# Performance work log

Hardware: AMD Instinct MI355X
Metric: run time of the kernel (lower is better)

The kernel has to match this reference:

```python
import jax, jax.numpy as jnp
import numpy as np

DILATIONS = [2 ** i for i in range(9)] * 3  # 27 layers
RD, SD, QD = 32, 512, 256


def conv1d(x, w, b, dilation=1, padding=0):
    # x: [B,C,T], w: [O,I,K], b: [O]
    out = jax.lax.conv_general_dilated(
        x, w, window_strides=(1,), padding=[(padding, padding)],
        rhs_dilation=(dilation,), dimension_numbers=('NCH', 'OIH', 'NCH'))
    return out + b[None, :, None]


def setup_inputs() -> dict:
    key = jax.random.key(0)
    ks = jax.random.split(key, 16)
    T = 131072
    L = len(DILATIONS)
    s = 0.05
    inp = {
        'x': jax.random.normal(ks[0], (1, 1, T), dtype=jnp.float32),
        'Wc': jax.random.normal(ks[1], (RD, 1, 3), dtype=jnp.float32) * s,
        'bc': jnp.zeros((RD,), dtype=jnp.float32),
        'Wt': jax.random.normal(ks[2], (L, RD, RD, 3), dtype=jnp.float32) * s,
        'bt': jnp.zeros((L, RD), dtype=jnp.float32),
        'Ws': jax.random.normal(ks[3], (L, RD, RD, 3), dtype=jnp.float32) * s,
        'bs': jnp.zeros((L, RD), dtype=jnp.float32),
        'Wskip': jax.random.normal(ks[4], (L, SD, RD, 1), dtype=jnp.float32) * s,
        'bskip': jnp.zeros((L, SD), dtype=jnp.float32),
        'Wdense': jax.random.normal(ks[5], (L, RD, RD, 1), dtype=jnp.float32) * s,
        'bdense': jnp.zeros((L, RD), dtype=jnp.float32),
        'Wp1': jax.random.normal(ks[6], (SD, SD, 1), dtype=jnp.float32) * s,
        'bp1': jnp.zeros((SD,), dtype=jnp.float32),
        'Wp2': jax.random.normal(ks[7], (QD, SD, 1), dtype=jnp.float32) * s,
        'bp2': jnp.zeros((QD,), dtype=jnp.float32),
    }
    return inp


def reference(x, Wc, bc, Wt, bt, Ws, bs, Wskip, bskip, Wdense, bdense, Wp1, bp1, Wp2, bp2):
    # causal conv: kernel 3, padding 1 (same length)
    x = conv1d(x, Wc, bc, dilation=1, padding=1)  # [1, RD, T]
    skip = jnp.zeros((1, SD, x.shape[2]), dtype=jnp.float32)
    for i, d in enumerate(DILATIONS):
        xin = x
        g = jnp.tanh(conv1d(x, Wt[i], bt[i], d, d)) * jax.nn.sigmoid(conv1d(x, Ws[i], bs[i], d, d))
        skip = skip + conv1d(g, Wskip[i], bskip[i])
        x = conv1d(g, Wdense[i], bdense[i]) + xin
    # NOTE: the original applies F.relu(x) on the residual path but then
    # overwrites x with the skip-path result, so that relu is dead code.
    out = conv1d(jax.nn.relu(conv1d(skip, Wp1, bp1)), Wp2, bp2)  # [1, QD, T]
    return jax.nn.log_softmax(out, axis=1)
```

## Files before the change

kernel.cpp:

```cpp
#include <hip/hip_runtime.h>

#define T_LEN 131072
#define RD 32
#define SD 512
#define QD 256
#define NL 27
#define KTOT (NL * RD)

typedef __attribute__((ext_vector_type(8))) short short8;
typedef __attribute__((ext_vector_type(4))) float floatx4;

__device__ __forceinline__ unsigned short f2bf(float f) {
    union { float f; unsigned int i; } v; v.f = f;
    unsigned int r = v.i + 0x7fffu + ((v.i >> 16) & 1u);
    return (unsigned short)(r >> 16);
}

__device__ __forceinline__ void gload_lds16(const void* g, void* l) {
    __builtin_amdgcn_global_load_lds(
        (const __attribute__((address_space(1))) unsigned int*)g,
        (__attribute__((address_space(3))) unsigned int*)l, 16, 0, 0);
}

__global__ __launch_bounds__(256)
void k_conv_init(const float* __restrict__ x, const float* __restrict__ Wc,
                 const float* __restrict__ bc, float* __restrict__ xout)
{
    const int t = blockIdx.x * 256 + threadIdx.x;
    const float xm = (t > 0) ? x[t - 1] : 0.f;
    const float x0 = x[t];
    const float xp = (t < T_LEN - 1) ? x[t + 1] : 0.f;
    float* row = xout + (size_t)t * RD;
#pragma unroll
    for (int o = 0; o < RD; ++o) {
        row[o] = bc[o] + Wc[o * 3 + 0] * xm + Wc[o * 3 + 1] * x0 + Wc[o * 3 + 2] * xp;
    }
}

__global__ __launch_bounds__(256)
void k_wprep(const float* __restrict__ Wt, const float* __restrict__ Ws,
             const float* __restrict__ Wd,
             unsigned short* __restrict__ Wg, unsigned short* __restrict__ Wdb)
{
    const int idx = blockIdx.x * 256 + threadIdx.x;
    const int n1 = NL * 64 * 96;
    const int n2 = NL * RD * RD;
    if (idx < n1) {
        const int l = idx / (64 * 96);
        const int rem = idx % (64 * 96);
        const int m = rem / 96;
        const int k = rem % 96;
        const int j = k / 32;
        const int c = k % 32;
        float v;
        if (m < 32) v = Wt[(((size_t)l * RD + m) * RD + c) * 3 + j];
        else        v = Ws[(((size_t)l * RD + (m - 32)) * RD + c) * 3 + j];
        Wg[idx] = f2bf(v);
    } else if (idx < n1 + n2) {
        const int i2 = idx - n1;
        Wdb[i2] = f2bf(Wd[i2]);
    }
}

__global__ __launch_bounds__(256)
void k_layer_mfma(const float* __restrict__ xin,
                  float* __restrict__ xout,
                  unsigned short* __restrict__ Gt,
                  const unsigned short* __restrict__ Wg,
                  const unsigned short* __restrict__ Wdb,
                  const float* __restrict__ bt, const float* __restrict__ bs,
                  const float* __restrict__ bd, int d, int layer)
{
    __shared__ unsigned short gtile[128 * 32];
    const int tid = threadIdx.x;
    const int lane = tid & 63;
    const int w = tid >> 6;
    const int quad = lane >> 4;
    const int l16 = lane & 15;
    const int tbase = blockIdx.x * 128 + w * 32;

    short8 afr[3][4];
#pragma unroll
    for (int j = 0; j < 3; ++j)
#pragma unroll
        for (int mt = 0; mt < 4; ++mt)
            afr[j][mt] = *reinterpret_cast<const short8*>(
                Wg + (size_t)(mt * 16 + l16) * 96 + j * 32 + quad * 8);

    floatx4 acc[4][2];
    const floatx4 vzero = {0.f, 0.f, 0.f, 0.f};
#pragma unroll
    for (int mt = 0; mt < 4; ++mt)
#pragma unroll
        for (int nt = 0; nt < 2; ++nt) acc[mt][nt] = vzero;

#pragma unroll
    for (int nt = 0; nt < 2; ++nt) {
        const int t = tbase + nt * 16 + l16;
#pragma unroll
        for (int j = 0; j < 3; ++j) {
            const int tt = t + (j - 1) * d;
            short8 b;
            if (tt >= 0 && tt < T_LEN) {
                const float* src = xin + (size_t)tt * RD + quad * 8;
                const floatx4 f0 = *reinterpret_cast<const floatx4*>(src);
                const floatx4 f1 = *reinterpret_cast<const floatx4*>(src + 4);
#pragma unroll
                for (int i = 0; i < 4; ++i) {
                    b[i] = (short)f2bf(f0[i]);
                    b[4 + i] = (short)f2bf(f1[i]);
                }
            } else {
#pragma unroll
                for (int i = 0; i < 8; ++i) b[i] = 0;
            }
#pragma unroll
            for (int mt = 0; mt < 4; ++mt)
                acc[mt][nt] = __builtin_amdgcn_mfma_f32_16x16x32_bf16(afr[j][mt], b, acc[mt][nt], 0, 0, 0);
        }
    }

#pragma unroll
    for (int nt = 0; nt < 2; ++nt) {
        const int t = tbase + nt * 16 + l16;
        const int tloc = w * 32 + nt * 16 + l16;
#pragma unroll
        for (int pair = 0; pair < 2; ++pair) {
            const floatx4 bt4 = *reinterpret_cast<const floatx4*>(bt + pair * 16 + quad * 4);
            const floatx4 bs4 = *reinterpret_cast<const floatx4*>(bs + pair * 16 + quad * 4);
            ushort4 u;
            unsigned short us[4];
#pragma unroll
            for (int r = 0; r < 4; ++r) {
                const float a1 = acc[pair][nt][r] + bt4[r];
                const float a2 = acc[2 + pair][nt][r] + bs4[r];
                const float th = 1.f - __fdividef(2.f, __expf(2.f * a1) + 1.f);
                const float sg = __fdividef(1.f, 1.f + __expf(-a2));
                us[r] = f2bf(th * sg);
            }
            u.x = us[0]; u.y = us[1]; u.z = us[2]; u.w = us[3];
            const int cbase = pair * 16 + quad * 4;
            *reinterpret_cast<ushort4*>(&gtile[tloc * 32 + cbase]) = u;
            *reinterpret_cast<ushort4*>(
                Gt + ((size_t)layer * T_LEN + t) * RD + cbase) = u;
        }
    }

    __syncthreads();

    short8 ad[2];
#pragma unroll
    for (int mt = 0; mt < 2; ++mt)
        ad[mt] = *reinterpret_cast<const short8*>(Wdb + (size_t)(mt * 16 + l16) * 32 + quad * 8);

#pragma unroll
    for (int nt = 0; nt < 2; ++nt) {
        const int t = tbase + nt * 16 + l16;
        const int tloc = w * 32 + nt * 16 + l16;
        const short8 bg = *reinterpret_cast<const short8*>(&gtile[tloc * 32 + quad * 8]);
#pragma unroll
        for (int mt = 0; mt < 2; ++mt) {
            const floatx4 a2 = __builtin_amdgcn_mfma_f32_16x16x32_bf16(ad[mt], bg, vzero, 0, 0, 0);
            const int m = mt * 16 + quad * 4;
            const floatx4 bd4 = *reinterpret_cast<const floatx4*>(bd + m);
            const floatx4 xi = *reinterpret_cast<const floatx4*>(xin + (size_t)t * RD + m);
            floatx4 o;
            o[0] = a2[0] + bd4[0] + xi[0];
            o[1] = a2[1] + bd4[1] + xi[1];
            o[2] = a2[2] + bd4[2] + xi[2];
            o[3] = a2[3] + bd4[3] + xi[3];
            *reinterpret_cast<floatx4*>(xout + (size_t)t * RD + m) = o;
        }
    }
}

__global__ __launch_bounds__(256)
void k_wcomb(const float* __restrict__ Wp1, const float* __restrict__ Wskip,
             unsigned short* __restrict__ Wcomb)
{
    const int idx = blockIdx.x * 256 + threadIdx.x;
    if (idx >= SD * KTOT) return;
    const int m = idx / KTOT;
    const int k = idx % KTOT;
    const int l = k / RD;
    const int c = k % RD;
    const float* wp1r = Wp1 + (size_t)m * SD;
    const float* wsk = Wskip + (size_t)l * SD * RD + c;
    float acc = 0.f;
    for (int j = 0; j < SD; ++j) acc += wp1r[j] * wsk[(size_t)j * RD];
    Wcomb[((size_t)l * SD + m) * RD + c] = f2bf(acc);
}

__global__ __launch_bounds__(512)
void k_hbias(const float* __restrict__ Wp1, const float* __restrict__ bp1,
             const float* __restrict__ bskip, float* __restrict__ hbias)
{
    __shared__ float sb[SD];
    const int tid = threadIdx.x;
    float s = 0.f;
    for (int l = 0; l < NL; ++l) s += bskip[l * SD + tid];
    sb[tid] = s;
    __syncthreads();
    float acc = bp1[tid];
    const float* r = Wp1 + (size_t)tid * SD;
    for (int j = 0; j < SD; ++j) acc += r[j] * sb[j];
    hbias[tid] = acc;
}

__global__ __launch_bounds__(256)
void k_cvt(const float* __restrict__ src, unsigned short* __restrict__ dst, int n)
{
    const int i = blockIdx.x * 256 + threadIdx.x;
    if (i < n) dst[i] = f2bf(src[i]);
}

__global__ __launch_bounds__(256)
void k_gemm1(const unsigned short* __restrict__ A,
             const unsigned short* __restrict__ B,
             const float* __restrict__ hbias,
             unsigned short* __restrict__ ht)
{
    __shared__ unsigned short ldsA[128 * 32];
    __shared__ unsigned short ldsB[128 * 32];
    const int tid = threadIdx.x;
    const int lane = tid & 63;
    const int w = tid >> 6;
    const int wm = w & 1;
    const int wn = w >> 1;
    const int quad = lane >> 4;
    const int l16 = lane & 15;

    const int g = blockIdx.x;
    const int m0 = ((g >> 3) & 3) * 128;
    const int n0 = ((g & 7) + 8 * (g >> 5)) * 128;

    const int r4 = lane >> 2;
    const int c4 = lane & 3;
    const int srcc = c4 ^ ((r4 >> 1) & 3);
    const int swz = (l16 >> 1) & 3;

    floatx4 acc[4][4];
    const floatx4 vzero = {0.f, 0.f, 0.f, 0.f};
#pragma unroll
    for (int mt = 0; mt < 4; ++mt)
#pragma unroll
        for (int nt = 0; nt < 4; ++nt) acc[mt][nt] = vzero;

    const unsigned short* pA = A + (size_t)(m0 + r4) * RD + srcc * 8;
    const unsigned short* pB = B + (size_t)(n0 + r4) * RD + srcc * 8;

    for (int kc = 0; kc < KTOT / 32; ++kc) {
#pragma unroll
        for (int c = 0; c < 2; ++c) {
            const int row = w * 32 + c * 16;
            gload_lds16(pA + ((size_t)kc * SD + row) * RD, &ldsA[(size_t)row * 32]);
            gload_lds16(pB + ((size_t)kc * T_LEN + row) * RD, &ldsB[(size_t)row * 32]);
        }
        __syncthreads();

        short8 afr[4], bfr[4];
#pragma unroll
        for (int mt = 0; mt < 4; ++mt)
            afr[mt] = *reinterpret_cast<const short8*>(
                &ldsA[(wm * 64 + mt * 16 + l16) * 32 + (quad ^ swz) * 8]);
#pragma unroll
        for (int nt = 0; nt < 4; ++nt)
            bfr[nt] = *reinterpret_cast<const short8*>(
                &ldsB[(wn * 64 + nt * 16 + l16) * 32 + (quad ^ swz) * 8]);
#pragma unroll
        for (int mt = 0; mt < 4; ++mt)
#pragma unroll
            for (int nt = 0; nt < 4; ++nt)
                acc[mt][nt] = __builtin_amdgcn_mfma_f32_16x16x32_bf16(afr[mt], bfr[nt], acc[mt][nt], 0, 0, 0);
        __syncthreads();
    }

#pragma unroll
    for (int mt = 0; mt < 4; ++mt) {
        const int m = m0 + wm * 64 + mt * 16 + quad * 4;
        const floatx4 hb = *reinterpret_cast<const floatx4*>(hbias + m);
        const size_t chunkbase = (size_t)(m >> 5) * T_LEN;
        const int mc = m & 31;
#pragma unroll
        for (int nt = 0; nt < 4; ++nt) {
            const int t = n0 + wn * 64 + nt * 16 + l16;
            ushort4 st;
            float v;
            v = acc[mt][nt][0] + hb[0]; st.x = f2bf(v > 0.f ? v : 0.f);
            v = acc[mt][nt][1] + hb[1]; st.y = f2bf(v > 0.f ? v : 0.f);
            v = acc[mt][nt][2] + hb[2]; st.z = f2bf(v > 0.f ? v : 0.f);
            v = acc[mt][nt][3] + hb[3]; st.w = f2bf(v > 0.f ? v : 0.f);
            *reinterpret_cast<ushort4*>(ht + (chunkbase + t) * RD + mc) = st;
        }
    }
}

__global__ __launch_bounds__(256)
void k_gemm2_lsm(const unsigned short* __restrict__ A,
                 const unsigned short* __restrict__ B,
                 const float* __restrict__ bp2,
                 float* __restrict__ out)
{
    __shared__ unsigned short ldsB[64 * 32];
    __shared__ float redmax[4 * 16 * 16];
    __shared__ float redsum[4 * 16 * 16];
    const int tid = threadIdx.x;
    const int lane = tid & 63;
    const int w = tid >> 6;
    const int quad = lane >> 4;
    const int l16 = lane & 15;
    const int m0 = w * 64;
    const int n0 = blockIdx.x * 64;

    const int r4 = lane >> 2;
    const int c4 = lane & 3;
    const int srcc = c4 ^ ((r4 >> 1) & 3);
    const int swz = (l16 >> 1) & 3;

    const unsigned short* ab[4];
#pragma unroll
    for (int mt = 0; mt < 4; ++mt)
        ab[mt] = A + (size_t)(m0 + mt * 16 + l16) * SD + quad * 8;

    const unsigned short* pB = B + (size_t)(n0 + w * 16 + r4) * RD + srcc * 8;

    floatx4 acc[4][4];
    const floatx4 vzero = {0.f, 0.f, 0.f, 0.f};
#pragma unroll
    for (int mt = 0; mt < 4; ++mt)
#pragma unroll
        for (int nt = 0; nt < 4; ++nt) acc[mt][nt] = vzero;

    for (int kc = 0; kc < SD / 32; ++kc) {
        const int k0 = kc * 32;
        gload_lds16(pB + (size_t)kc * T_LEN * RD, &ldsB[(size_t)(w * 16) * 32]);
        short8 afr[4];
#pragma unroll
        for (int mt = 0; mt < 4; ++mt)
            afr[mt] = *reinterpret_cast<const short8*>(ab[mt] + k0);
        __syncthreads();

        short8 bfr[4];
#pragma unroll
        for (int nt = 0; nt < 4; ++nt)
            bfr[nt] = *reinterpret_cast<const short8*>(
                &ldsB[(nt * 16 + l16) * 32 + (quad ^ swz) * 8]);
#pragma unroll
        for (int mt = 0; mt < 4; ++mt)
#pragma unroll
            for (int nt = 0; nt < 4; ++nt)
                acc[mt][nt] = __builtin_amdgcn_mfma_f32_16x16x32_bf16(
                    afr[mt], bfr[nt], acc[mt][nt], 0, 0, 0);
        __syncthreads();
    }

#pragma unroll
    for (int mt = 0; mt < 4; ++mt) {
        const int mb = m0 + mt * 16 + quad * 4;
        const floatx4 bz = *reinterpret_cast<const floatx4*>(bp2 + mb);
#pragma unroll
        for (int nt = 0; nt < 4; ++nt)
#pragma unroll
            for (int j = 0; j < 4; ++j) acc[mt][nt][j] += bz[j];
    }

#pragma unroll
    for (int nt = 0; nt < 4; ++nt) {
        float lm = -1e30f;
#pragma unroll
        for (int mt = 0; mt < 4; ++mt)
#pragma unroll
            for (int j = 0; j < 4; ++j) lm = fmaxf(lm, acc[mt][nt][j]);
        redmax[nt * 256 + l16 * 16 + w * 4 + quad] = lm;
    }
    __syncthreads();

    float lse[4];
#pragma unroll
    for (int nt = 0; nt < 4; ++nt) {
        float gm = -1e30f;
#pragma unroll
        for (int i = 0; i < 16; ++i) gm = fmaxf(gm, redmax[nt * 256 + l16 * 16 + i]);
        float ls = 0.f;
#pragma unroll
        for (int mt = 0; mt < 4; ++mt)
#pragma unroll
            for (int j = 0; j < 4; ++j) ls += __expf(acc[mt][nt][j] - gm);
        redsum[nt * 256 + l16 * 16 + w * 4 + quad] = ls;
        lse[nt] = gm;
    }
    __syncthreads();

#pragma unroll
    for (int nt = 0; nt < 4; ++nt) {
        float tot = 0.f;
#pragma unroll
        for (int i = 0; i < 16; ++i) tot += redsum[nt * 256 + l16 * 16 + i];
        lse[nt] = lse[nt] + __logf(tot);
    }

#pragma unroll
    for (int mt = 0; mt < 4; ++mt) {
        const int mb = m0 + mt * 16 + quad * 4;
#pragma unroll
        for (int nt = 0; nt < 4; ++nt) {
            const int t = n0 + nt * 16 + l16;
#pragma unroll
            for (int j = 0; j < 4; ++j)
                out[(size_t)(mb + j) * T_LEN + t] = acc[mt][nt][j] - lse[nt];
        }
    }
}

extern "C" void kernel_launch(void* const* d_in, const int* in_sizes, int n_in,
                              void* d_out, int out_size, void* d_ws, size_t ws_size,
                              hipStream_t stream)
{
    (void)in_sizes; (void)n_in; (void)out_size; (void)ws_size;
    const float* x     = (const float*)d_in[0];
    const float* Wc    = (const float*)d_in[1];
    const float* bc    = (const float*)d_in[2];
    const float* Wt    = (const float*)d_in[3];
    const float* bt    = (const float*)d_in[4];
    const float* Ws    = (const float*)d_in[5];
    const float* bs    = (const float*)d_in[6];
    const float* Wskip = (const float*)d_in[7];
    const float* bskip = (const float*)d_in[8];
    const float* Wd    = (const float*)d_in[9];
    const float* bd    = (const float*)d_in[10];
    const float* Wp1   = (const float*)d_in[11];
    const float* bp1   = (const float*)d_in[12];
    const float* Wp2   = (const float*)d_in[13];
    const float* bp2   = (const float*)d_in[14];
    float* out = (float*)d_out;

    char* p = (char*)d_ws;
    unsigned short* Gt = (unsigned short*)p;    p += (size_t)T_LEN * KTOT * 2;
    unsigned short* ht = (unsigned short*)p;    p += (size_t)T_LEN * SD * 2;
    unsigned short* Wcomb = (unsigned short*)p; p += (size_t)SD * KTOT * 2;
    unsigned short* Wp2b = (unsigned short*)p;  p += (size_t)QD * SD * 2;
    unsigned short* Wg = (unsigned short*)p;    p += (size_t)NL * 64 * 96 * 2;
    unsigned short* Wdb = (unsigned short*)p;   p += (size_t)NL * RD * RD * 2;
    float* hbias = (float*)p;                   p += (size_t)SD * 4;

    char* q = (char*)ht;
    float* xa = (float*)q;                      q += (size_t)T_LEN * RD * 4;
    float* xb = (float*)q;                      q += (size_t)T_LEN * RD * 4;

    k_wcomb<<<(SD * KTOT + 255) / 256, 256, 0, stream>>>(Wp1, Wskip, Wcomb);
    k_hbias<<<1, 512, 0, stream>>>(Wp1, bp1, bskip, hbias);
    k_cvt<<<(QD * SD + 255) / 256, 256, 0, stream>>>(Wp2, Wp2b, QD * SD);
    {
        const int nprep = NL * 64 * 96 + NL * RD * RD;
        k_wprep<<<(nprep + 255) / 256, 256, 0, stream>>>(Wt, Ws, Wd, Wg, Wdb);
    }
    k_conv_init<<<T_LEN / 256, 256, 0, stream>>>(x, Wc, bc, xa);

    static const int dil[NL] = {1, 2, 4, 8, 16, 32, 64, 128, 256,
                                1, 2, 4, 8, 16, 32, 64, 128, 256,
                                1, 2, 4, 8, 16, 32, 64, 128, 256};
    const float* cur = xa;
    float* nxt = xb;
    for (int i = 0; i < NL; ++i) {
        k_layer_mfma<<<T_LEN / 128, 256, 0, stream>>>(
            cur, nxt, Gt,
            Wg + (size_t)i * 64 * 96,
            Wdb + (size_t)i * RD * RD,
            bt + (size_t)i * RD,
            bs + (size_t)i * RD,
            bd + (size_t)i * RD,
            dil[i], i);
        float* tf = (float*)cur; cur = nxt; nxt = tf;
    }

    k_gemm1<<<4 * (T_LEN / 128), 256, 0, stream>>>(Wcomb, Gt, hbias, ht);
    k_gemm2_lsm<<<T_LEN / 64, 256, 0, stream>>>(Wp2b, ht, bp2, out);
}
```

Baseline: 1.029 ms.

## Fuse all residual layers into one persistent kernel with neighbor flag sync

Replaces the 27 per-layer kernel launches with a single persistent kernel of 512 blocks. Each block walks all layers over its own 256-timestep chunk and waits only on per-layer completion flags from its two neighbouring blocks, which is enough because the largest dilation does not exceed the chunk size. This is meant to remove the launch gaps and full-grid barriers between layers, and it also skips the unused dense residual update in the last layer. In exchange it depends on every block being resident at once, since spinning blocks would otherwise deadlock, and it adds flag polling and memory fences.

```diff
diff --git a/kernel.cpp b/kernel.cpp
--- a/kernel.cpp
+++ b/kernel.cpp
@@ -6,6 +6,8 @@
 #define QD 256
 #define NL 27
 #define KTOT (NL * RD)
+#define GRID_F 512
+#define CHUNK 256
 
 typedef __attribute__((ext_vector_type(8))) short short8;
 typedef __attribute__((ext_vector_type(4))) float floatx4;
@@ -24,8 +26,11 @@
 
 __global__ __launch_bounds__(256)
 void k_conv_init(const float* __restrict__ x, const float* __restrict__ Wc,
-                 const float* __restrict__ bc, float* __restrict__ xout)
-{
+                 const float* __restrict__ bc, float* __restrict__ xout,
+                 int* __restrict__ flags)
+{
+    if (threadIdx.x < NL) flags[(size_t)threadIdx.x * GRID_F + blockIdx.x] = 0;
+
     const int t = blockIdx.x * 256 + threadIdx.x;
     const float xm = (t > 0) ? x[t - 1] : 0.f;
     const float x0 = x[t];
@@ -62,114 +67,158 @@
     }
 }
 
-__global__ __launch_bounds__(256)
-void k_layer_mfma(const float* __restrict__ xin,
-                  float* __restrict__ xout,
-                  unsigned short* __restrict__ Gt,
-                  const unsigned short* __restrict__ Wg,
-                  const unsigned short* __restrict__ Wdb,
-                  const float* __restrict__ bt, const float* __restrict__ bs,
-                  const float* __restrict__ bd, int d, int layer)
-{
+__global__ __launch_bounds__(256, 2)
+void k_layers_fused(const float* __restrict__ x0,
+                    float* __restrict__ xa, float* __restrict__ xb,
+                    unsigned short* __restrict__ Gt,
+                    const unsigned short* __restrict__ WgAll,
+                    const unsigned short* __restrict__ WdbAll,
+                    const float* __restrict__ btAll,
+                    const float* __restrict__ bsAll,
+                    const float* __restrict__ bdAll,
+                    int* __restrict__ flags)
+{
+    static const int dil[NL] = {1, 2, 4, 8, 16, 32, 64, 128, 256,
+                                1, 2, 4, 8, 16, 32, 64, 128, 256,
+                                1, 2, 4, 8, 16, 32, 64, 128, 256};
     __shared__ unsigned short gtile[128 * 32];
+    const int b = blockIdx.x;
     const int tid = threadIdx.x;
     const int lane = tid & 63;
     const int w = tid >> 6;
     const int quad = lane >> 4;
     const int l16 = lane & 15;
-    const int tbase = blockIdx.x * 128 + w * 32;
-
-    short8 afr[3][4];
-#pragma unroll
-    for (int j = 0; j < 3; ++j)
-#pragma unroll
-        for (int mt = 0; mt < 4; ++mt)
-            afr[j][mt] = *reinterpret_cast<const short8*>(
-                Wg + (size_t)(mt * 16 + l16) * 96 + j * 32 + quad * 8);
-
-    floatx4 acc[4][2];
     const floatx4 vzero = {0.f, 0.f, 0.f, 0.f};
-#pragma unroll
-    for (int mt = 0; mt < 4; ++mt)
-#pragma unroll
-        for (int nt = 0; nt < 2; ++nt) acc[mt][nt] = vzero;
-
-#pragma unroll
-    for (int nt = 0; nt < 2; ++nt) {
-        const int t = tbase + nt * 16 + l16;
-#pragma unroll
-        for (int j = 0; j < 3; ++j) {
-            const int tt = t + (j - 1) * d;
-            short8 b;
-            if (tt >= 0 && tt < T_LEN) {
-                const float* src = xin + (size_t)tt * RD + quad * 8;
-                const floatx4 f0 = *reinterpret_cast<const floatx4*>(src);
-                const floatx4 f1 = *reinterpret_cast<const floatx4*>(src + 4);
-#pragma unroll
-                for (int i = 0; i < 4; ++i) {
-                    b[i] = (short)f2bf(f0[i]);
-                    b[4 + i] = (short)f2bf(f1[i]);
+
+    for (int l = 0; l < NL; ++l) {
+        const int d = dil[l];
+        const float* xin = (l == 0) ? x0 : ((l & 1) ? xa : xb);
+        float* xout = (l & 1) ? xb : xa;
+        const unsigned short* Wg = WgAll + (size_t)l * 64 * 96;
+        const unsigned short* Wdb = WdbAll + (size_t)l * RD * RD;
+        const float* bt = btAll + (size_t)l * RD;
+        const float* bs = bsAll + (size_t)l * RD;
+        const float* bd = bdAll + (size_t)l * RD;
+
+        if (l > 0) {
+            if (tid == 0) {
+                if (b > 0)
+                    while (__hip_atomic_load(&flags[(size_t)(l - 1) * GRID_F + b - 1],
+                                             __ATOMIC_RELAXED, __HIP_MEMORY_SCOPE_AGENT) == 0)
+                        __builtin_amdgcn_s_sleep(1);
+                if (b < GRID_F - 1)
+                    while (__hip_atomic_load(&flags[(size_t)(l - 1) * GRID_F + b + 1],
+                                             __ATOMIC_RELAXED, __HIP_MEMORY_SCOPE_AGENT) == 0)
+                        __builtin_amdgcn_s_sleep(1);
+                __threadfence();
+            }
+            __syncthreads();
+        }
+
+        short8 afr[3][4];
+#pragma unroll
+        for (int j = 0; j < 3; ++j)
+#pragma unroll
+            for (int mt = 0; mt < 4; ++mt)
+                afr[j][mt] = *reinterpret_cast<const short8*>(
+                    Wg + (size_t)(mt * 16 + l16) * 96 + j * 32 + quad * 8);
+
+        short8 ad[2];
+#pragma unroll
+        for (int mt = 0; mt < 2; ++mt)
+            ad[mt] = *reinterpret_cast<const short8*>(Wdb + (size_t)(mt * 16 + l16) * 32 + quad * 8);
+
+        for (int st = 0; st < 2; ++st) {
+            const int tbase = b * CHUNK + st * 128 + w * 32;
+
+            floatx4 acc[4][2];
+#pragma unroll
+            for (int mt = 0; mt < 4; ++mt)
+#pragma unroll
+                for (int nt = 0; nt < 2; ++nt) acc[mt][nt] = vzero;
+
+#pragma unroll
+            for (int nt = 0; nt < 2; ++nt) {
+                const int t = tbase + nt * 16 + l16;
+#pragma unroll
+                for (int j = 0; j < 3; ++j) {
+                    const int tt = t + (j - 1) * d;
+                    short8 bb;
+                    if (tt >= 0 && tt < T_LEN) {
+                        const float* src = xin + (size_t)tt * RD + quad * 8;
+                        const floatx4 f0 = *reinterpret_cast<const floatx4*>(src);
+                        const floatx4 f1 = *reinterpret_cast<const floatx4*>(src + 4);
+#pragma unroll
+                        for (int i = 0; i < 4; ++i) {
+                            bb[i] = (short)f2bf(f0[i]);
+                            bb[4 + i] = (short)f2bf(f1[i]);
+                        }
+                    } else {
+#pragma unroll
+                        for (int i = 0; i < 8; ++i) bb[i] = 0;
+                    }
+#pragma unroll
+                    for (int mt = 0; mt < 4; ++mt)
+                        acc[mt][nt] = __builtin_amdgcn_mfma_f32_16x16x32_bf16(afr[j][mt], bb, acc[mt][nt], 0, 0, 0);
                 }
-            } else {
-#pragma unroll
-                for (int i = 0; i < 8; ++i) b[i] = 0;
             }
-#pragma unroll
-            for (int mt = 0; mt < 4; ++mt)
-                acc[mt][nt] = __builtin_amdgcn_mfma_f32_16x16x32_bf16(afr[j][mt], b, acc[mt][nt], 0, 0, 0);
+
+#pragma unroll
+            for (int nt = 0; nt < 2; ++nt) {
+                const int t = tbase + nt * 16 + l16;
+                const int tloc = w * 32 + nt * 16 + l16;
+#pragma unroll
+                for (int pair = 0; pair < 2; ++pair) {
+                    const floatx4 bt4 = *reinterpret_cast<const floatx4*>(bt + pair * 16 + quad * 4);
+                    const floatx4 bs4 = *reinterpret_cast<const floatx4*>(bs + pair * 16 + quad * 4);
+                    ushort4 u;
+                    unsigned short us[4];
+#pragma unroll
+                    for (int r = 0; r < 4; ++r) {
+                        const float a1 = acc[pair][nt][r] + bt4[r];
+                        const float a2 = acc[2 + pair][nt][r] + bs4[r];
+                        const float th = 1.f - __fdividef(2.f, __expf(2.f * a1) + 1.f);
+                        const float sg = __fdividef(1.f, 1.f + __expf(-a2));
+                        us[r] = f2bf(th * sg);
+                    }
+                    u.x = us[0]; u.y = us[1]; u.z = us[2]; u.w = us[3];
+                    const int cbase = pair * 16 + quad * 4;
+                    *reinterpret_cast<ushort4*>(&gtile[tloc * 32 + cbase]) = u;
+                    *reinterpret_cast<ushort4*>(
+                        Gt + ((size_t)l * T_LEN + t) * RD + cbase) = u;
+                }
+            }
+
+            __syncthreads();
+
+            if (l < NL - 1) {
+#pragma unroll
+                for (int nt = 0; nt < 2; ++nt) {
+                    const int t = tbase + nt * 16 + l16;
+                    const int tloc = w * 32 + nt * 16 + l16;
+                    const short8 bg = *reinterpret_cast<const short8*>(&gtile[tloc * 32 + quad * 8]);
+#pragma unroll
+                    for (int mt = 0; mt < 2; ++mt) {
+                        const floatx4 a2 = __builtin_amdgcn_mfma_f32_16x16x32_bf16(ad[mt], bg, vzero, 0, 0, 0);
+                        const int m = mt * 16 + quad * 4;
+                        const floatx4 bd4 = *reinterpret_cast<const floatx4*>(bd + m);
+                        const floatx4 xi = *reinterpret_cast<const floatx4*>(xin + (size_t)t * RD + m);
+                        floatx4 o;
+                        o[0] = a2[0] + bd4[0] + xi[0];
+                        o[1] = a2[1] + bd4[1] + xi[1];
+                        o[2] = a2[2] + bd4[2] + xi[2];
+                        o[3] = a2[3] + bd4[3] + xi[3];
+                        *reinterpret_cast<floatx4*>(xout + (size_t)t * RD + m) = o;
+                    }
+                }
+            }
+            __syncthreads();
         }
-    }
-
-#pragma unroll
-    for (int nt = 0; nt < 2; ++nt) {
-        const int t = tbase + nt * 16 + l16;
-        const int tloc = w * 32 + nt * 16 + l16;
-#pragma unroll
-        for (int pair = 0; pair < 2; ++pair) {
-            const floatx4 bt4 = *reinterpret_cast<const floatx4*>(bt + pair * 16 + quad * 4);
-            const floatx4 bs4 = *reinterpret_cast<const floatx4*>(bs + pair * 16 + quad * 4);
-            ushort4 u;
-            unsigned short us[4];
-#pragma unroll
-            for (int r = 0; r < 4; ++r) {
-                const float a1 = acc[pair][nt][r] + bt4[r];
-                const float a2 = acc[2 + pair][nt][r] + bs4[r];
-                const float th = 1.f - __fdividef(2.f, __expf(2.f * a1) + 1.f);
-                const float sg = __fdividef(1.f, 1.f + __expf(-a2));
-                us[r] = f2bf(th * sg);
-            }
-            u.x = us[0]; u.y = us[1]; u.z = us[2]; u.w = us[3];
-            const int cbase = pair * 16 + quad * 4;
-            *reinterpret_cast<ushort4*>(&gtile[tloc * 32 + cbase]) = u;
-            *reinterpret_cast<ushort4*>(
-                Gt + ((size_t)layer * T_LEN + t) * RD + cbase) = u;
-        }
-    }
-
-    __syncthreads();
-
-    short8 ad[2];
-#pragma unroll
-    for (int mt = 0; mt < 2; ++mt)
-        ad[mt] = *reinterpret_cast<const short8*>(Wdb + (size_t)(mt * 16 + l16) * 32 + quad * 8);
-
-#pragma unroll
-    for (int nt = 0; nt < 2; ++nt) {
-        const int t = tbase + nt * 16 + l16;
-        const int tloc = w * 32 + nt * 16 + l16;
-        const short8 bg = *reinterpret_cast<const short8*>(&gtile[tloc * 32 + quad * 8]);
-#pragma unroll
-        for (int mt = 0; mt < 2; ++mt) {
-            const floatx4 a2 = __builtin_amdgcn_mfma_f32_16x16x32_bf16(ad[mt], bg, vzero, 0, 0, 0);
-            const int m = mt * 16 + quad * 4;
-            const floatx4 bd4 = *reinterpret_cast<const floatx4*>(bd + m);
-            const floatx4 xi = *reinterpret_cast<const floatx4*>(xin + (size_t)t * RD + m);
-            floatx4 o;
-            o[0] = a2[0] + bd4[0] + xi[0];
-            o[1] = a2[1] + bd4[1] + xi[1];
-            o[2] = a2[2] + bd4[2] + xi[2];
-            o[3] = a2[3] + bd4[3] + xi[3];
-            *reinterpret_cast<floatx4*>(xout + (size_t)t * RD + m) = o;
+
+        if (l < NL - 1 && tid == 0) {
+            __threadfence();
+            __hip_atomic_store(&flags[(size_t)l * GRID_F + b], 1,
+                               __ATOMIC_RELEASE, __HIP_MEMORY_SCOPE_AGENT);
         }
     }
 }
@@ -442,8 +491,10 @@
     unsigned short* Wg = (unsigned short*)p;    p += (size_t)NL * 64 * 96 * 2;
     unsigned short* Wdb = (unsigned short*)p;   p += (size_t)NL * RD * RD * 2;
     float* hbias = (float*)p;                   p += (size_t)SD * 4;
+    int* flags = (int*)p;                       p += (size_t)NL * GRID_F * 4;
 
     char* q = (char*)ht;
+    float* x0 = (float*)q;                      q += (size_t)T_LEN * RD * 4;
     float* xa = (float*)q;                      q += (size_t)T_LEN * RD * 4;
     float* xb = (float*)q;                      q += (size_t)T_LEN * RD * 4;
 
@@ -454,24 +505,10 @@
         const int nprep = NL * 64 * 96 + NL * RD * RD;
         k_wprep<<<(nprep + 255) / 256, 256, 0, stream>>>(Wt, Ws, Wd, Wg, Wdb);
     }
-    k_conv_init<<<T_LEN / 256, 256, 0, stream>>>(x, Wc, bc, xa);
-
-    static const int dil[NL] = {1, 2, 4, 8, 16, 32, 64, 128, 256,
-                                1, 2, 4, 8, 16, 32, 64, 128, 256,
-                                1, 2, 4, 8, 16, 32, 64, 128, 256};
-    const float* cur = xa;
-    float* nxt = xb;
-    for (int i = 0; i < NL; ++i) {
-        k_layer_mfma<<<T_LEN / 128, 256, 0, stream>>>(
-            cur, nxt, Gt,
-            Wg + (size_t)i * 64 * 96,
-            Wdb + (size_t)i * RD * RD,
-            bt + (size_t)i * RD,
-            bs + (size_t)i * RD,
-            bd + (size_t)i * RD,
-            dil[i], i);
-        float* tf = (float*)cur; cur = nxt; nxt = tf;
-    }
+    k_conv_init<<<T_LEN / 256, 256, 0, stream>>>(x, Wc, bc, x0, flags);
+
+    k_layers_fused<<<GRID_F, 256, 0, stream>>>(
+        x0, xa, xb, Gt, Wg, Wdb, bt, bs, bd, flags);
 
     k_gemm1<<<4 * (T_LEN / 128), 256, 0, stream>>>(Wcomb, Gt, hbias, ht);
     k_gemm2_lsm<<<T_LEN / 64, 256, 0, stream>>>(Wp2b, ht, bp2, out);
```

After: 2.563 ms. 2.49x slower.

## Fuse first seven dilated layers per stack into one LDS-resident halo kernel

Applied to the files above, without the earlier changes.

Adds a kernel that keeps a 512-step window of the residual stream in shared memory and runs layers with dilations 1 through 64 back to back. Each block recomputes a 128-step halo on both sides so it needs no inter-block exchange. The aim is to cut the per-layer global read and write of the fp32 residual and the launch count; only the dilation-128 and dilation-256 layers still use the per-layer kernel. The cost is doubled gate and dense compute on halo rows. About 144KB of shared memory per block likely limits each CU to one 512-thread block, so occupancy drops.

```diff
diff --git a/kernel.cpp b/kernel.cpp
--- a/kernel.cpp
+++ b/kernel.cpp
@@ -6,6 +6,11 @@
 #define QD 256
 #define NL 27
 #define KTOT (NL * RD)
+
+#define GC 256
+#define GH 128
+#define GR 512
+#define GNL 7
 
 typedef __attribute__((ext_vector_type(8))) short short8;
 typedef __attribute__((ext_vector_type(4))) float floatx4;
@@ -62,6 +67,168 @@
     }
 }
 
+__global__ __launch_bounds__(512, 2)
+void k_group7(const float* __restrict__ xin_g, float* __restrict__ xout_g,
+              unsigned short* __restrict__ Gt,
+              const unsigned short* __restrict__ WgAll,
+              const unsigned short* __restrict__ WdbAll,
+              const float* __restrict__ btAll,
+              const float* __restrict__ bsAll,
+              const float* __restrict__ bdAll,
+              int l0)
+{
+    __shared__ float xs[2][GR * RD];
+    __shared__ unsigned short gtile[256 * RD];
+
+    const int tid = threadIdx.x;
+    const int lane = tid & 63;
+    const int w = tid >> 6;
+    const int quad = lane >> 4;
+    const int l16 = lane & 15;
+    const int b = blockIdx.x;
+    const int t0 = b * GC;
+    const floatx4 vzero = {0.f, 0.f, 0.f, 0.f};
+
+    {
+        const int e = tid;
+        const int t = t0 - GH + e;
+        float* dst = &xs[0][e * RD];
+        if (t >= 0 && t < T_LEN) {
+            const float* src = xin_g + (size_t)t * RD;
+#pragma unroll
+            for (int c = 0; c < 8; ++c)
+                *reinterpret_cast<floatx4*>(&dst[(c ^ (e & 7)) * 4]) =
+                    *reinterpret_cast<const floatx4*>(src + c * 4);
+        } else {
+#pragma unroll
+            for (int c = 0; c < 8; ++c)
+                *reinterpret_cast<floatx4*>(&dst[(c ^ (e & 7)) * 4]) = vzero;
+        }
+    }
+    __syncthreads();
+
+    int cur = 0;
+    for (int i = 0; i < GNL; ++i) {
+        const int d = 1 << i;
+        const int l = l0 + i;
+        const unsigned short* Wg = WgAll + (size_t)l * 64 * 96;
+        const unsigned short* Wdb = WdbAll + (size_t)l * RD * RD;
+        const float* btp = btAll + (size_t)l * RD;
+        const float* bsp = bsAll + (size_t)l * RD;
+        const float* bdp = bdAll + (size_t)l * RD;
+
+        short8 afr[3][4];
+#pragma unroll
+        for (int j = 0; j < 3; ++j)
+#pragma unroll
+            for (int mt = 0; mt < 4; ++mt)
+                afr[j][mt] = *reinterpret_cast<const short8*>(
+                    Wg + (size_t)(mt * 16 + l16) * 96 + j * 32 + quad * 8);
+        short8 ad[2];
+#pragma unroll
+        for (int mt = 0; mt < 2; ++mt)
+            ad[mt] = *reinterpret_cast<const short8*>(
+                Wdb + (size_t)(mt * 16 + l16) * RD + quad * 8);
+
+        for (int rs = 0; rs < GR; rs += 256) {
+            const int rloc = w * 32;
+
+            floatx4 acc[4][2];
+#pragma unroll
+            for (int mt = 0; mt < 4; ++mt)
+#pragma unroll
+                for (int nt = 0; nt < 2; ++nt) acc[mt][nt] = vzero;
+
+#pragma unroll
+            for (int nt = 0; nt < 2; ++nt) {
+                const int e = rs + rloc + nt * 16 + l16;
+#pragma unroll
+                for (int j = 0; j < 3; ++j) {
+                    const int et = e + (j - 1) * d;
+                    short8 bb;
+                    if (et >= 0 && et < GR) {
+                        const float* srow = &xs[cur][et * RD];
+                        const int sw = et & 7;
+                        const floatx4 f0 = *reinterpret_cast<const floatx4*>(
+                            &srow[((2 * quad) ^ sw) * 4]);
+                        const floatx4 f1 = *reinterpret_cast<const floatx4*>(
+                            &srow[(((2 * quad) + 1) ^ sw) * 4]);
+#pragma unroll
+                        for (int k2 = 0; k2 < 4; ++k2) {
+                            bb[k2] = (short)f2bf(f0[k2]);
+                            bb[4 + k2] = (short)f2bf(f1[k2]);
+                        }
+                    } else {
+#pragma unroll
+                        for (int k2 = 0; k2 < 8; ++k2) bb[k2] = 0;
+                    }
+#pragma unroll
+                    for (int mt = 0; mt < 4; ++mt)
+                        acc[mt][nt] = __builtin_amdgcn_mfma_f32_16x16x32_bf16(
+                            afr[j][mt], bb, acc[mt][nt], 0, 0, 0);
+                }
+            }
+
+#pragma unroll
+            for (int nt = 0; nt < 2; ++nt) {
+                const int tloc = rloc + nt * 16 + l16;
+                const int e = rs + tloc;
+#pragma unroll
+                for (int pair = 0; pair < 2; ++pair) {
+                    const floatx4 bt4 = *reinterpret_cast<const floatx4*>(btp + pair * 16 + quad * 4);
+                    const floatx4 bs4 = *reinterpret_cast<const floatx4*>(bsp + pair * 16 + quad * 4);
+                    ushort4 u;
+                    unsigned short us[4];
+#pragma unroll
+                    for (int r = 0; r < 4; ++r) {
+                        const float a1 = acc[pair][nt][r] + bt4[r];
+                        const float a2 = acc[2 + pair][nt][r] + bs4[r];
+                        const float th = 1.f - __fdividef(2.f, __expf(2.f * a1) + 1.f);
+                        const float sg = __fdividef(1.f, 1.f + __expf(-a2));
+                        us[r] = f2bf(th * sg);
+                    }
+                    u.x = us[0]; u.y = us[1]; u.z = us[2]; u.w = us[3];
+                    const int cbase = pair * 16 + quad * 4;
+                    *reinterpret_cast<ushort4*>(&gtile[tloc * RD + cbase]) = u;
+                    if (e >= GH && e < GH + GC) {
+                        const int t = t0 + e - GH;
+                        *reinterpret_cast<ushort4*>(
+                            Gt + ((size_t)l * T_LEN + t) * RD + cbase) = u;
+                    }
+                }
+            }
+
+            __syncthreads();
+
+#pragma unroll
+            for (int nt = 0; nt < 2; ++nt) {
+                const int tloc = rloc + nt * 16 + l16;
+                const int e = rs + tloc;
+                const int t = t0 + e - GH;
+                const bool inT = (t >= 0 && t < T_LEN);
+                const short8 bg = *reinterpret_cast<const short8*>(&gtile[tloc * RD + quad * 8]);
+#pragma unroll
+                for (int mt = 0; mt < 2; ++mt) {
+                    const floatx4 a2v = __builtin_amdgcn_mfma_f32_16x16x32_bf16(ad[mt], bg, vzero, 0, 0, 0);
+                    const int m = mt * 16 + quad * 4;
+                    const int pos = ((4 * mt + quad) ^ (e & 7)) * 4;
+                    const floatx4 bd4 = *reinterpret_cast<const floatx4*>(bdp + m);
+                    const floatx4 xi = *reinterpret_cast<const floatx4*>(&xs[cur][e * RD + pos]);
+                    floatx4 o;
+#pragma unroll
+                    for (int r = 0; r < 4; ++r)
+                        o[r] = inT ? (a2v[r] + bd4[r] + xi[r]) : 0.f;
+                    *reinterpret_cast<floatx4*>(&xs[cur ^ 1][e * RD + pos]) = o;
+                    if (i == GNL - 1 && e >= GH && e < GH + GC)
+                        *reinterpret_cast<floatx4*>(xout_g + (size_t)t * RD + m) = o;
+                }
+            }
+            __syncthreads();
+        }
+        cur ^= 1;
+    }
+}
+
 __global__ __launch_bounds__(256)
 void k_layer_mfma(const float* __restrict__ xin,
                   float* __restrict__ xout,
@@ -456,21 +623,30 @@
     }
     k_conv_init<<<T_LEN / 256, 256, 0, stream>>>(x, Wc, bc, xa);
 
-    static const int dil[NL] = {1, 2, 4, 8, 16, 32, 64, 128, 256,
-                                1, 2, 4, 8, 16, 32, 64, 128, 256,
-                                1, 2, 4, 8, 16, 32, 64, 128, 256};
     const float* cur = xa;
     float* nxt = xb;
-    for (int i = 0; i < NL; ++i) {
+    for (int s = 0; s < 3; ++s) {
+        k_group7<<<T_LEN / GC, 512, 0, stream>>>(
+            cur, nxt, Gt, Wg, Wdb, bt, bs, bd, 9 * s);
+        { float* tf = (float*)cur; cur = nxt; nxt = tf; }
         k_layer_mfma<<<T_LEN / 128, 256, 0, stream>>>(
             cur, nxt, Gt,
-            Wg + (size_t)i * 64 * 96,
-            Wdb + (size_t)i * RD * RD,
-            bt + (size_t)i * RD,
-            bs + (size_t)i * RD,
-            bd + (size_t)i * RD,
-            dil[i], i);
-        float* tf = (float*)cur; cur = nxt; nxt = tf;
+            Wg + (size_t)(9 * s + 7) * 64 * 96,
+            Wdb + (size_t)(9 * s + 7) * RD * RD,
+            bt + (size_t)(9 * s + 7) * RD,
+            bs + (size_t)(9 * s + 7) * RD,
+            bd + (size_t)(9 * s + 7) * RD,
+            128, 9 * s + 7);
+        { float* tf = (float*)cur; cur = nxt; nxt = tf; }
+        k_layer_mfma<<<T_LEN / 128, 256, 0, stream>>>(
+            cur, nxt, Gt,
+            Wg + (size_t)(9 * s + 8) * 64 * 96,
+            Wdb + (size_t)(9 * s + 8) * RD * RD,
+            bt + (size_t)(9 * s + 8) * RD,
+            bs + (size_t)(9 * s + 8) * RD,
+            bd + (size_t)(9 * s + 8) * RD,
+            256, 9 * s + 8);
+        { float* tf = (float*)cur; cur = nxt; nxt = tf; }
     }
 
     k_gemm1<<<4 * (T_LEN / 128), 256, 0, stream>>>(Wcomb, Gt, hbias, ht);
```

After: 1.045 ms. Within noise of the previous version (+1.5%).

## Stage layer inputs in LDS via async loads with bf16 shadow and zero-padded halos

Applied to the files above, without the earlier changes.

Each layer now also writes a bf16 copy of the residual stream, and reads its three dilated taps through async global-to-LDS loads from that bf16 copy. Zero-padded guard rows replace the per-tap bounds checks, and the fp32 center rows are staged in LDS with XOR swizzles to avoid bank conflicts. The last layer skips the dense residual update it does not need. In exchange every layer writes an extra bf16 buffer and uses more LDS per block, which may limit occupancy.

```diff
diff --git a/kernel.cpp b/kernel.cpp
--- a/kernel.cpp
+++ b/kernel.cpp
@@ -6,6 +6,7 @@
 #define QD 256
 #define NL 27
 #define KTOT (NL * RD)
+#define GPAD 256
 
 typedef __attribute__((ext_vector_type(8))) short short8;
 typedef __attribute__((ext_vector_type(4))) float floatx4;
@@ -24,16 +25,38 @@
 
 __global__ __launch_bounds__(256)
 void k_conv_init(const float* __restrict__ x, const float* __restrict__ Wc,
-                 const float* __restrict__ bc, float* __restrict__ xout)
-{
-    const int t = blockIdx.x * 256 + threadIdx.x;
+                 const float* __restrict__ bc,
+                 float* __restrict__ xaG, unsigned short* __restrict__ xabG,
+                 float* __restrict__ xbG, unsigned short* __restrict__ xbbG)
+{
+    const int gid = blockIdx.x * 256 + threadIdx.x;
+
+    if (gid < 4 * GPAD * RD) {
+        const int region = gid >> 13;
+        const int idx = gid & (GPAD * RD - 1);
+        float* fg; unsigned short* hg;
+        const size_t post = (size_t)(GPAD + T_LEN) * RD;
+        switch (region) {
+            case 0:  fg = xaG;        hg = xabG;        break;
+            case 1:  fg = xaG + post; hg = xabG + post; break;
+            case 2:  fg = xbG;        hg = xbbG;        break;
+            default: fg = xbG + post; hg = xbbG + post; break;
+        }
+        fg[idx] = 0.f;
+        hg[idx] = 0;
+    }
+
+    const int t = gid;
     const float xm = (t > 0) ? x[t - 1] : 0.f;
     const float x0 = x[t];
     const float xp = (t < T_LEN - 1) ? x[t + 1] : 0.f;
-    float* row = xout + (size_t)t * RD;
+    float* row = xaG + (size_t)(GPAD + t) * RD;
+    unsigned short* rowb = xabG + (size_t)(GPAD + t) * RD;
 #pragma unroll
     for (int o = 0; o < RD; ++o) {
-        row[o] = bc[o] + Wc[o * 3 + 0] * xm + Wc[o * 3 + 1] * x0 + Wc[o * 3 + 2] * xp;
+        const float v = bc[o] + Wc[o * 3 + 0] * xm + Wc[o * 3 + 1] * x0 + Wc[o * 3 + 2] * xp;
+        row[o] = v;
+        rowb[o] = f2bf(v);
     }
 }
 
@@ -62,22 +85,53 @@
     }
 }
 
-__global__ __launch_bounds__(256)
-void k_layer_mfma(const float* __restrict__ xin,
-                  float* __restrict__ xout,
-                  unsigned short* __restrict__ Gt,
-                  const unsigned short* __restrict__ Wg,
-                  const unsigned short* __restrict__ Wdb,
-                  const float* __restrict__ bt, const float* __restrict__ bs,
-                  const float* __restrict__ bd, int d, int layer)
-{
-    __shared__ unsigned short gtile[128 * 32];
+__global__ __launch_bounds__(256, 3)
+void k_layer_stage(const float* __restrict__ xin,
+                   const unsigned short* __restrict__ xinb,
+                   float* __restrict__ xout,
+                   unsigned short* __restrict__ xoutb,
+                   unsigned short* __restrict__ Gt,
+                   const unsigned short* __restrict__ Wg,
+                   const unsigned short* __restrict__ Wdb,
+                   const float* __restrict__ bt, const float* __restrict__ bs,
+                   const float* __restrict__ bd, int d, int layer)
+{
+    __shared__ unsigned short bandsL[3][128 * 32];
+    __shared__ float centerL[128 * 32];
+    __shared__ unsigned short gtileL[128 * 32];
+
     const int tid = threadIdx.x;
     const int lane = tid & 63;
     const int w = tid >> 6;
     const int quad = lane >> 4;
     const int l16 = lane & 15;
-    const int tbase = blockIdx.x * 128 + w * 32;
+    const int rbase = w * 32;
+    const bool last = (layer == NL - 1);
+    const floatx4 vzero = {0.f, 0.f, 0.f, 0.f};
+
+    const int r16c = lane >> 2;
+    const int scB = (lane & 3) ^ ((lane >> 3) & 3);
+    const int r8c = lane >> 3;
+    const int scC = (lane & 7) ^ r8c;
+    const long long gbase = (long long)blockIdx.x * 128 + rbase;
+
+#pragma unroll
+    for (int j = 0; j < 3; ++j) {
+        const long long b0 = gbase + (long long)(j - 1) * d;
+#pragma unroll
+        for (int i = 0; i < 2; ++i)
+            gload_lds16(xinb + (b0 + i * 16 + r16c) * RD + scB * 8,
+                        &bandsL[j][(rbase + i * 16) * 32]);
+    }
+    if (!last) {
+#pragma unroll
+        for (int i = 0; i < 4; ++i)
+            gload_lds16(xin + (gbase + i * 8 + r8c) * RD + scC * 4,
+                        &centerL[(rbase + i * 8) * 32]);
+        asm volatile("s_waitcnt vmcnt(4)" ::: "memory");
+    } else {
+        asm volatile("s_waitcnt vmcnt(0)" ::: "memory");
+    }
 
     short8 afr[3][4];
 #pragma unroll
@@ -88,7 +142,6 @@
                 Wg + (size_t)(mt * 16 + l16) * 96 + j * 32 + quad * 8);
 
     floatx4 acc[4][2];
-    const floatx4 vzero = {0.f, 0.f, 0.f, 0.f};
 #pragma unroll
     for (int mt = 0; mt < 4; ++mt)
 #pragma unroll
@@ -96,34 +149,26 @@
 
 #pragma unroll
     for (int nt = 0; nt < 2; ++nt) {
-        const int t = tbase + nt * 16 + l16;
+        const int rloc = rbase + nt * 16 + l16;
+        const int key2 = (rloc >> 1) & 3;
 #pragma unroll
         for (int j = 0; j < 3; ++j) {
-            const int tt = t + (j - 1) * d;
-            short8 b;
-            if (tt >= 0 && tt < T_LEN) {
-                const float* src = xin + (size_t)tt * RD + quad * 8;
-                const floatx4 f0 = *reinterpret_cast<const floatx4*>(src);
-                const floatx4 f1 = *reinterpret_cast<const floatx4*>(src + 4);
-#pragma unroll
-                for (int i = 0; i < 4; ++i) {
-                    b[i] = (short)f2bf(f0[i]);
-                    b[4 + i] = (short)f2bf(f1[i]);
-                }
-            } else {
-#pragma unroll
-                for (int i = 0; i < 8; ++i) b[i] = 0;
-            }
+            const short8 bb = *reinterpret_cast<const short8*>(
+                &bandsL[j][rloc * 32 + ((quad ^ key2) * 8)]);
 #pragma unroll
             for (int mt = 0; mt < 4; ++mt)
-                acc[mt][nt] = __builtin_amdgcn_mfma_f32_16x16x32_bf16(afr[j][mt], b, acc[mt][nt], 0, 0, 0);
-        }
-    }
+                acc[mt][nt] = __builtin_amdgcn_mfma_f32_16x16x32_bf16(
+                    afr[j][mt], bb, acc[mt][nt], 0, 0, 0);
+        }
+    }
+
+    if (!last) asm volatile("s_waitcnt vmcnt(0)" ::: "memory");
 
 #pragma unroll
     for (int nt = 0; nt < 2; ++nt) {
-        const int t = tbase + nt * 16 + l16;
-        const int tloc = w * 32 + nt * 16 + l16;
+        const int rloc = rbase + nt * 16 + l16;
+        const int key2 = (rloc >> 1) & 3;
+        const long long t = (long long)blockIdx.x * 128 + rloc;
 #pragma unroll
         for (int pair = 0; pair < 2; ++pair) {
             const floatx4 bt4 = *reinterpret_cast<const floatx4*>(bt + pair * 16 + quad * 4);
@@ -140,36 +185,48 @@
             }
             u.x = us[0]; u.y = us[1]; u.z = us[2]; u.w = us[3];
             const int cbase = pair * 16 + quad * 4;
-            *reinterpret_cast<ushort4*>(&gtile[tloc * 32 + cbase]) = u;
+            if (!last) {
+                const int colS = (pair * 2 + (quad >> 1)) ^ key2;
+                *reinterpret_cast<ushort4*>(
+                    &gtileL[rloc * 32 + colS * 8 + (quad & 1) * 4]) = u;
+            }
             *reinterpret_cast<ushort4*>(
                 Gt + ((size_t)layer * T_LEN + t) * RD + cbase) = u;
         }
     }
 
-    __syncthreads();
-
-    short8 ad[2];
-#pragma unroll
-    for (int mt = 0; mt < 2; ++mt)
-        ad[mt] = *reinterpret_cast<const short8*>(Wdb + (size_t)(mt * 16 + l16) * 32 + quad * 8);
-
-#pragma unroll
-    for (int nt = 0; nt < 2; ++nt) {
-        const int t = tbase + nt * 16 + l16;
-        const int tloc = w * 32 + nt * 16 + l16;
-        const short8 bg = *reinterpret_cast<const short8*>(&gtile[tloc * 32 + quad * 8]);
-#pragma unroll
-        for (int mt = 0; mt < 2; ++mt) {
-            const floatx4 a2 = __builtin_amdgcn_mfma_f32_16x16x32_bf16(ad[mt], bg, vzero, 0, 0, 0);
-            const int m = mt * 16 + quad * 4;
-            const floatx4 bd4 = *reinterpret_cast<const floatx4*>(bd + m);
-            const floatx4 xi = *reinterpret_cast<const floatx4*>(xin + (size_t)t * RD + m);
-            floatx4 o;
-            o[0] = a2[0] + bd4[0] + xi[0];
-            o[1] = a2[1] + bd4[1] + xi[1];
-            o[2] = a2[2] + bd4[2] + xi[2];
-            o[3] = a2[3] + bd4[3] + xi[3];
-            *reinterpret_cast<floatx4*>(xout + (size_t)t * RD + m) = o;
+    if (!last) {
+        short8 ad[2];
+#pragma unroll
+        for (int mt = 0; mt < 2; ++mt)
+            ad[mt] = *reinterpret_cast<const short8*>(
+                Wdb + (size_t)(mt * 16 + l16) * RD + quad * 8);
+
+#pragma unroll
+        for (int nt = 0; nt < 2; ++nt) {
+            const int rloc = rbase + nt * 16 + l16;
+            const int key2 = (rloc >> 1) & 3;
+            const long long t = (long long)blockIdx.x * 128 + rloc;
+            const short8 bg = *reinterpret_cast<const short8*>(
+                &gtileL[rloc * 32 + ((quad ^ key2) * 8)]);
+#pragma unroll
+            for (int mt = 0; mt < 2; ++mt) {
+                const floatx4 a2v = __builtin_amdgcn_mfma_f32_16x16x32_bf16(
+                    ad[mt], bg, vzero, 0, 0, 0);
+                const int m = mt * 16 + quad * 4;
+                const int c16 = (mt * 4 + quad) ^ (rloc & 7);
+                const floatx4 xi = *reinterpret_cast<const floatx4*>(
+                    &centerL[rloc * 32 + c16 * 4]);
+                const floatx4 bd4 = *reinterpret_cast<const floatx4*>(bd + m);
+                floatx4 o;
+                ushort4 ob;
+                o[0] = a2v[0] + bd4[0] + xi[0]; ob.x = f2bf(o[0]);
+                o[1] = a2v[1] + bd4[1] + xi[1]; ob.y = f2bf(o[1]);
+                o[2] = a2v[2] + bd4[2] + xi[2]; ob.z = f2bf(o[2]);
+                o[3] = a2v[3] + bd4[3] + xi[3]; ob.w = f2bf(o[3]);
+                *reinterpret_cast<floatx4*>(xout + (size_t)t * RD + m) = o;
+                *reinterpret_cast<ushort4*>(xoutb + (size_t)t * RD + m) = ob;
+            }
         }
     }
 }
@@ -444,8 +501,15 @@
     float* hbias = (float*)p;                   p += (size_t)SD * 4;
 
     char* q = (char*)ht;
-    float* xa = (float*)q;                      q += (size_t)T_LEN * RD * 4;
-    float* xb = (float*)q;                      q += (size_t)T_LEN * RD * 4;
+    const size_t grows = (size_t)(T_LEN + 2 * GPAD) * RD;
+    float* xaG = (float*)q;                     q += grows * 4;
+    float* xbG = (float*)q;                     q += grows * 4;
+    unsigned short* xabG = (unsigned short*)q;  q += grows * 2;
+    unsigned short* xbbG = (unsigned short*)q;  q += grows * 2;
+    float* xa = xaG + (size_t)GPAD * RD;
+    float* xb = xbG + (size_t)GPAD * RD;
+    unsigned short* xab = xabG + (size_t)GPAD * RD;
+    unsigned short* xbb = xbbG + (size_t)GPAD * RD;
 
     k_wcomb<<<(SD * KTOT + 255) / 256, 256, 0, stream>>>(Wp1, Wskip, Wcomb);
     k_hbias<<<1, 512, 0, stream>>>(Wp1, bp1, bskip, hbias);
@@ -454,23 +518,26 @@
         const int nprep = NL * 64 * 96 + NL * RD * RD;
         k_wprep<<<(nprep + 255) / 256, 256, 0, stream>>>(Wt, Ws, Wd, Wg, Wdb);
     }
-    k_conv_init<<<T_LEN / 256, 256, 0, stream>>>(x, Wc, bc, xa);
+    k_conv_init<<<T_LEN / 256, 256, 0, stream>>>(x, Wc, bc, xaG, xabG, xbG, xbbG);
 
     static const int dil[NL] = {1, 2, 4, 8, 16, 32, 64, 128, 256,
                                 1, 2, 4, 8, 16, 32, 64, 128, 256,
                                 1, 2, 4, 8, 16, 32, 64, 128, 256};
     const float* cur = xa;
+    const unsigned short* curb = xab;
     float* nxt = xb;
+    unsigned short* nxtb = xbb;
     for (int i = 0; i < NL; ++i) {
-        k_layer_mfma<<<T_LEN / 128, 256, 0, stream>>>(
-            cur, nxt, Gt,
+        k_layer_stage<<<T_LEN / 128, 256, 0, stream>>>(
+            cur, curb, nxt, nxtb, Gt,
             Wg + (size_t)i * 64 * 96,
             Wdb + (size_t)i * RD * RD,
             bt + (size_t)i * RD,
             bs + (size_t)i * RD,
             bd + (size_t)i * RD,
             dil[i], i);
-        float* tf = (float*)cur; cur = nxt; nxt = tf;
+        { float* tf = (float*)cur; cur = nxt; nxt = tf; }
+        { unsigned short* tb = (unsigned short*)curb; curb = nxtb; nxtb = tb; }
     }
 
     k_gemm1<<<4 * (T_LEN / 128), 256, 0, stream>>>(Wcomb, Gt, hbias, ht);
```

Measured after the change: 1.016 ms. About the same (-1.3%).
